# Kernel optimization log

Measured on AMD Instinct MI355X. Metric: run time of the kernel, lower is better.

## Reference

```python
import jax, jax.numpy as jnp
import numpy as np

EMBED_DIM = 1024
NUM_HEADS = 16
HEAD_DIM = EMBED_DIM // NUM_HEADS


def setup_inputs() -> dict:
    key = jax.random.key(0)
    ks = jax.random.split(key, 5)
    B, N, E = 2, 2048, EMBED_DIM
    scale = E ** -0.5
    return {
        "x": jax.random.normal(ks[0], (B, N, E), dtype=jnp.float32),
        "w_qkv": jax.random.normal(ks[1], (E, 3 * E), dtype=jnp.float32) * scale,
        "b_qkv": jnp.zeros((3 * E,), dtype=jnp.float32),
        "w_proj": jax.random.normal(ks[2], (E, E), dtype=jnp.float32) * scale,
        "b_proj": jnp.zeros((E,), dtype=jnp.float32),
    }


def reference(x, w_qkv, b_qkv, w_proj, b_proj):
    B, N, E = x.shape
    H, D = NUM_HEADS, HEAD_DIM
    qkv = x @ w_qkv + b_qkv                      # [B,N,3E]
    qkv = qkv.reshape(B, N, 3, H, D)
    q = qkv[:, :, 0].transpose(0, 2, 1, 3)        # [B,H,N,D]
    k = qkv[:, :, 1].transpose(0, 2, 1, 3)
    v = qkv[:, :, 2].transpose(0, 2, 1, 3)
    attn = jnp.einsum('bhnd,bhmd->bhnm', q, k) * (D ** -0.5)
    attn = jax.nn.softmax(attn, axis=-1)          # dropout is identity in eval mode
    out = jnp.einsum('bhnm,bhmd->bhnd', attn, v)  # [B,H,N,D]
    out = out.transpose(0, 2, 1, 3).reshape(B, N, E)
    return out @ w_proj + b_proj
```

## Files before the change

### kernel.cpp

```cpp
#include <hip/hip_runtime.h>
#include <hip/hip_bf16.h>
#include <cstdint>
#include <cstddef>


typedef __attribute__((ext_vector_type(8))) short short8;
typedef __attribute__((ext_vector_type(4))) short short4v;
typedef __attribute__((ext_vector_type(4))) float f32x4;

#define MFMA16(a, b, c) __builtin_amdgcn_mfma_f32_16x16x32_bf16((a), (b), (c), 0, 0, 0)

__device__ __forceinline__ float b2f(short s) {
  union { unsigned u; float f; } x; x.u = ((unsigned)(unsigned short)s) << 16; return x.f;
}
__device__ __forceinline__ short f2b(float f) {
  union { float f; unsigned u; } x; x.f = f;
  unsigned r = x.u + 0x7fffu + ((x.u >> 16) & 1u);
  return (short)(r >> 16);
}
__device__ __forceinline__ void async_lds16(const void* g, void* l) {
  __builtin_amdgcn_global_load_lds(
      (const __attribute__((address_space(1))) void*)g,
      (__attribute__((address_space(3))) void*)l, 16, 0, 0);
}

__global__ __launch_bounds__(256) void cast_f32_bf16(const float* __restrict__ in,
                                                     short* __restrict__ out, int n4) {
  int idx = blockIdx.x * 256 + threadIdx.x;
  if (idx < n4) {
    f32x4 v = ((const f32x4*)in)[idx];
    short4v o;
    #pragma unroll
    for (int e = 0; e < 4; ++e) o[e] = f2b(v[e]);
    ((short4v*)out)[idx] = o;
  }
}

__global__ __launch_bounds__(256) void transpose_cast(const float* __restrict__ in,
                                                      short* __restrict__ out,
                                                      int R, int C) {
  __shared__ float tile[32][33];
  int c0 = blockIdx.x * 32, r0 = blockIdx.y * 32;
  int tx = threadIdx.x, ty = threadIdx.y;
  #pragma unroll
  for (int i = ty; i < 32; i += 8)
    tile[i][tx] = in[(size_t)(r0 + i) * C + c0 + tx];
  __syncthreads();
  #pragma unroll
  for (int i = ty; i < 32; i += 8)
    out[(size_t)(c0 + i) * R + r0 + tx] = f2b(tile[tx][i]);
}

__global__ __launch_bounds__(256) void gemm_qkv(const short* __restrict__ xb,
                                                const short* __restrict__ wT,
                                                const float* __restrict__ bias,
                                                short* __restrict__ Qb,
                                                short* __restrict__ Kb,
                                                short* __restrict__ Vt) {
  __shared__ short lds_a[128 * 32];
  __shared__ short lds_b[128 * 32];
  const int tid = threadIdx.x, wid = tid >> 6, lane = tid & 63;
  const int lg = lane >> 4, lr = lane & 15;
  const int m0 = blockIdx.x * 128, n0 = blockIdx.y * 128;
  const int wr = wid >> 1, wc = wid & 1;
  const int K = 1024;

  f32x4 acc[4][4];
  #pragma unroll
  for (int i = 0; i < 4; ++i)
    #pragma unroll
    for (int j = 0; j < 4; ++j) acc[i][j] = (f32x4)0.0f;

  for (int k0 = 0; k0 < K; k0 += 32) {
    #pragma unroll
    for (int it = 0; it < 2; ++it) {
      int chunk = it * 256 + tid;
      int row = chunk >> 2, kc = (chunk & 3) * 8;
      async_lds16(xb + (size_t)(m0 + row) * K + k0 + kc, lds_a + chunk * 8);
      async_lds16(wT + (size_t)(n0 + row) * K + k0 + kc, lds_b + chunk * 8);
    }
    __syncthreads();
    short8 af[4], bfr[4];
    #pragma unroll
    for (int i = 0; i < 4; ++i)
      af[i] = *(const short8*)&lds_a[(wr * 64 + i * 16 + lr) * 32 + lg * 8];
    #pragma unroll
    for (int j = 0; j < 4; ++j)
      bfr[j] = *(const short8*)&lds_b[(wc * 64 + j * 16 + lr) * 32 + lg * 8];
    #pragma unroll
    for (int i = 0; i < 4; ++i)
      #pragma unroll
      for (int j = 0; j < 4; ++j) acc[i][j] = MFMA16(af[i], bfr[j], acc[i][j]);
    __syncthreads();
  }

  #pragma unroll
  for (int i = 0; i < 4; ++i) {
    int gm = m0 + wr * 64 + i * 16 + lg * 4;
    int bb = gm >> 11, n = gm & 2047;
    #pragma unroll
    for (int j = 0; j < 4; ++j) {
      int gc = n0 + wc * 64 + j * 16 + lr;
      float bv = bias[gc];
      int which = gc >> 10;
      int h = (gc >> 6) & 15;
      int dd = gc & 63;
      size_t qkbase = ((size_t)((bb * 16 + h) * 2048 + n)) * 64 + dd;
      if (which == 2) {
        size_t vtbase = ((size_t)((bb * 16 + h) * 64 + dd)) * 2048 + n;
        short4v pv;
        #pragma unroll
        for (int r = 0; r < 4; ++r) pv[r] = f2b(acc[i][j][r] + bv);
        *(short4v*)&Vt[vtbase] = pv;
      } else {
        short* dst = (which == 0) ? Qb : Kb;
        #pragma unroll
        for (int r = 0; r < 4; ++r)
          dst[qkbase + (size_t)r * 64] = f2b(acc[i][j][r] + bv);
      }
    }
  }
}

__global__ __launch_bounds__(512) void attn_fwd(const short* __restrict__ Qb,
                                                const short* __restrict__ Kb,
                                                const short* __restrict__ Vt,
                                                short* __restrict__ aob) {
  __shared__ short k_lds[64 * 64];
  __shared__ short v_lds[64 * 64];
  __shared__ short p_lds[8 * 16 * 64];
  const int tid = threadIdx.x, wid = tid >> 6, lane = tid & 63;
  const int lg = lane >> 4, lr = lane & 15;
  const int bh = blockIdx.x, qt = blockIdx.y;
  const int q0 = qt * 128 + wid * 16;
  const short* Qbh = Qb + (size_t)bh * 2048 * 64;
  const short* Kbh = Kb + (size_t)bh * 2048 * 64;
  const short* Vbh = Vt + (size_t)bh * 64 * 2048;
  const int rm = (lr >> 1) & 7;

  short8 qf[2];
  #pragma unroll
  for (int kk = 0; kk < 2; ++kk) {
    qf[kk] = *(const short8*)(Qbh + (size_t)(q0 + lr) * 64 + kk * 32 + lg * 8);
    #pragma unroll
    for (int e = 0; e < 8; ++e) qf[kk][e] = f2b(b2f(qf[kk][e]) * 0.125f);
  }

  f32x4 o[4];
  #pragma unroll
  for (int dt = 0; dt < 4; ++dt) o[dt] = (f32x4)0.0f;
  float m_ = -__builtin_inff(), l_ = 0.0f;

  for (int kv0 = 0; kv0 < 2048; kv0 += 64) {
    {
      int row = tid >> 3;
      int src = ((tid & 7) ^ ((row >> 1) & 7)) * 8;
      async_lds16(Kbh + (size_t)(kv0 + row) * 64 + src, k_lds + tid * 8);
      async_lds16(Vbh + (size_t)row * 2048 + kv0 + src, v_lds + tid * 8);
    }
    __syncthreads();

    f32x4 s[4];
    #pragma unroll
    for (int jt = 0; jt < 4; ++jt) s[jt] = (f32x4)0.0f;
    #pragma unroll
    for (int jt = 0; jt < 4; ++jt)
      #pragma unroll
      for (int kk = 0; kk < 2; ++kk) {
        short8 kf = *(const short8*)&k_lds[(jt * 16 + lr) * 64 +
                                           (((kk * 4 + lg) ^ rm) * 8)];
        s[jt] = MFMA16(kf, qf[kk], s[jt]);
      }

    float mx = s[0][0];
    #pragma unroll
    for (int jt = 0; jt < 4; ++jt)
      #pragma unroll
      for (int r = 0; r < 4; ++r) mx = fmaxf(mx, s[jt][r]);
    mx = fmaxf(mx, __shfl_xor(mx, 16));
    mx = fmaxf(mx, __shfl_xor(mx, 32));
    float mn = fmaxf(m_, mx);
    float corr = __expf(m_ - mn);
    m_ = mn;
    float ps = 0.0f;
    #pragma unroll
    for (int jt = 0; jt < 4; ++jt)
      #pragma unroll
      for (int r = 0; r < 4; ++r) {
        float p = __expf(s[jt][r] - mn);
        s[jt][r] = p;
        ps += p;
      }
    ps += __shfl_xor(ps, 16);
    ps += __shfl_xor(ps, 32);
    l_ = l_ * corr + ps;
    #pragma unroll
    for (int dt = 0; dt < 4; ++dt)
      #pragma unroll
      for (int r = 0; r < 4; ++r) o[dt][r] *= corr;

    #pragma unroll
    for (int jt = 0; jt < 4; ++jt) {
      short4v pv;
      #pragma unroll
      for (int r = 0; r < 4; ++r) pv[r] = f2b(s[jt][r]);
      *(short4v*)&p_lds[wid * 1024 + lr * 64 +
                        (((jt * 2 + (lg >> 1)) ^ rm) * 8) + (lg & 1) * 4] = pv;
    }
    asm volatile("s_waitcnt lgkmcnt(0)" ::: "memory");
    __builtin_amdgcn_sched_barrier(0);

    #pragma unroll
    for (int kk = 0; kk < 2; ++kk) {
      short8 pa = *(const short8*)&p_lds[wid * 1024 + lr * 64 +
                                         (((kk * 4 + lg) ^ rm) * 8)];
      #pragma unroll
      for (int dt = 0; dt < 4; ++dt) {
        short8 vb = *(const short8*)&v_lds[(dt * 16 + lr) * 64 +
                                           (((kk * 4 + lg) ^ rm) * 8)];
        o[dt] = MFMA16(vb, pa, o[dt]);
      }
    }
    __syncthreads();
  }

  const int bb = bh >> 4, h = bh & 15;
  const float inv_l = __frcp_rn(l_);
  #pragma unroll
  for (int dt = 0; dt < 4; ++dt) {
    short4v ov;
    #pragma unroll
    for (int r = 0; r < 4; ++r) ov[r] = f2b(o[dt][r] * inv_l);
    *(short4v*)&aob[(size_t)(bb * 2048 + q0 + lr) * 1024 + h * 64 + dt * 16 + lg * 4] = ov;
  }
}

__global__ __launch_bounds__(256) void gemm_proj(const short* __restrict__ aob,
                                                 const short* __restrict__ wT,
                                                 const float* __restrict__ bias,
                                                 float* __restrict__ out) {
  __shared__ short lds_a[128 * 32];
  __shared__ short lds_b[128 * 32];
  const int tid = threadIdx.x, wid = tid >> 6, lane = tid & 63;
  const int lg = lane >> 4, lr = lane & 15;
  const int m0 = blockIdx.x * 128, n0 = blockIdx.y * 128;
  const int wr = wid >> 1, wc = wid & 1;
  const int K = 1024;

  f32x4 acc[4][4];
  #pragma unroll
  for (int i = 0; i < 4; ++i)
    #pragma unroll
    for (int j = 0; j < 4; ++j) acc[i][j] = (f32x4)0.0f;

  for (int k0 = 0; k0 < K; k0 += 32) {
    #pragma unroll
    for (int it = 0; it < 2; ++it) {
      int chunk = it * 256 + tid;
      int row = chunk >> 2, kc = (chunk & 3) * 8;
      async_lds16(aob + (size_t)(m0 + row) * K + k0 + kc, lds_a + chunk * 8);
      async_lds16(wT + (size_t)(n0 + row) * K + k0 + kc, lds_b + chunk * 8);
    }
    __syncthreads();
    short8 af[4], bfr[4];
    #pragma unroll
    for (int i = 0; i < 4; ++i)
      af[i] = *(const short8*)&lds_a[(wr * 64 + i * 16 + lr) * 32 + lg * 8];
    #pragma unroll
    for (int j = 0; j < 4; ++j)
      bfr[j] = *(const short8*)&lds_b[(wc * 64 + j * 16 + lr) * 32 + lg * 8];
    #pragma unroll
    for (int i = 0; i < 4; ++i)
      #pragma unroll
      for (int j = 0; j < 4; ++j) acc[i][j] = MFMA16(af[i], bfr[j], acc[i][j]);
    __syncthreads();
  }

  #pragma unroll
  for (int i = 0; i < 4; ++i) {
    int gm = m0 + wr * 64 + i * 16 + lg * 4;
    #pragma unroll
    for (int j = 0; j < 4; ++j) {
      int gc = n0 + wc * 64 + j * 16 + lr;
      float bv = bias[gc];
      #pragma unroll
      for (int r = 0; r < 4; ++r)
        out[(size_t)(gm + r) * 1024 + gc] = acc[i][j][r] + bv;
    }
  }
}

extern "C" void kernel_launch(void* const* d_in, const int* in_sizes, int n_in,
                              void* d_out, int out_size, void* d_ws, size_t ws_size,
                              hipStream_t stream) {
  const float* x     = (const float*)d_in[0];
  const float* wqkv  = (const float*)d_in[1];
  const float* bqkv  = (const float*)d_in[2];
  const float* wproj = (const float*)d_in[3];
  const float* bproj = (const float*)d_in[4];
  float* out = (float*)d_out;

  char* ws = (char*)d_ws;
  short* xb     = (short*)ws; ws += (size_t)4096 * 1024 * 2;
  short* wqkvT  = (short*)ws; ws += (size_t)3072 * 1024 * 2;
  short* wprojT = (short*)ws; ws += (size_t)1024 * 1024 * 2;
  short* Qb     = (short*)ws; ws += (size_t)32 * 2048 * 64 * 2;
  short* Kb     = (short*)ws; ws += (size_t)32 * 2048 * 64 * 2;
  short* Vt     = (short*)ws; ws += (size_t)32 * 64 * 2048 * 2;
  short* aob    = (short*)ws; ws += (size_t)4096 * 1024 * 2;

  cast_f32_bf16<<<4096, 256, 0, stream>>>(x, xb, 4096 * 1024 / 4);
  transpose_cast<<<dim3(96, 32), dim3(32, 8), 0, stream>>>(wqkv, wqkvT, 1024, 3072);
  transpose_cast<<<dim3(32, 32), dim3(32, 8), 0, stream>>>(wproj, wprojT, 1024, 1024);
  gemm_qkv<<<dim3(32, 24), 256, 0, stream>>>(xb, wqkvT, bqkv, Qb, Kb, Vt);
  attn_fwd<<<dim3(32, 16), 512, 0, stream>>>(Qb, Kb, Vt, aob);
  gemm_proj<<<dim3(32, 8), 256, 0, stream>>>(aob, wprojT, bproj, out);
}
```

Baseline: 221.8 us.

## Double-buffer attention K/V, use exp2 with lazy rescale, swizzle blocks, shrink proj tile

The attention kernel now double-buffers the K/V tiles in LDS so the next tile's async load overlaps compute. Softmax uses exp2 with log2e folded into the Q scale, and the running max is only rescaled when it grows by more than a threshold. All three GEMM/attention kernels remap block IDs with an XCD-style swizzle, and the projection GEMM uses 64x128 tiles to launch more blocks. These target memory-load latency, transcendental cost, and load balance across XCDs, at the cost of more LDS and some numerical slack from deferred rescaling.

New measurement: 214.5 us. 3.3% less time.

```diff
diff --git a/kernel.cpp b/kernel.cpp
--- a/kernel.cpp
+++ b/kernel.cpp
@@ -9,6 +9,7 @@
 typedef __attribute__((ext_vector_type(4))) float f32x4;
 
 #define MFMA16(a, b, c) __builtin_amdgcn_mfma_f32_16x16x32_bf16((a), (b), (c), 0, 0, 0)
+#define EXP2F(x) __builtin_amdgcn_exp2f(x)
 
 __device__ __forceinline__ float b2f(short s) {
   union { unsigned u; float f; } x; x.u = ((unsigned)(unsigned short)s) << 16; return x.f;
@@ -61,7 +62,9 @@
   __shared__ short lds_b[128 * 32];
   const int tid = threadIdx.x, wid = tid >> 6, lane = tid & 63;
   const int lg = lane >> 4, lr = lane & 15;
-  const int m0 = blockIdx.x * 128, n0 = blockIdx.y * 128;
+  const int lin = blockIdx.x;
+  const int swz = (lin & 7) * 96 + (lin >> 3);
+  const int m0 = (swz & 31) * 128, n0 = (swz >> 5) * 128;
   const int wr = wid >> 1, wc = wid & 1;
   const int K = 1024;
 
@@ -126,24 +129,29 @@
                                                 const short* __restrict__ Kb,
                                                 const short* __restrict__ Vt,
                                                 short* __restrict__ aob) {
-  __shared__ short k_lds[64 * 64];
-  __shared__ short v_lds[64 * 64];
+  __shared__ short k_lds[2][64 * 64];
+  __shared__ short v_lds[2][64 * 64];
   __shared__ short p_lds[8 * 16 * 64];
   const int tid = threadIdx.x, wid = tid >> 6, lane = tid & 63;
   const int lg = lane >> 4, lr = lane & 15;
-  const int bh = blockIdx.x, qt = blockIdx.y;
+  const int lin = blockIdx.x;
+  const int swz = (lin & 7) * 64 + (lin >> 3);
+  const int qt = swz & 15, bh = swz >> 4;
   const int q0 = qt * 128 + wid * 16;
   const short* Qbh = Qb + (size_t)bh * 2048 * 64;
   const short* Kbh = Kb + (size_t)bh * 2048 * 64;
   const short* Vbh = Vt + (size_t)bh * 64 * 2048;
   const int rm = (lr >> 1) & 7;
 
+  const int srow = tid >> 3;
+  const int ssrc = ((tid & 7) ^ ((srow >> 1) & 7)) * 8;
+
   short8 qf[2];
   #pragma unroll
   for (int kk = 0; kk < 2; ++kk) {
     qf[kk] = *(const short8*)(Qbh + (size_t)(q0 + lr) * 64 + kk * 32 + lg * 8);
     #pragma unroll
-    for (int e = 0; e < 8; ++e) qf[kk][e] = f2b(b2f(qf[kk][e]) * 0.125f);
+    for (int e = 0; e < 8; ++e) qf[kk][e] = f2b(b2f(qf[kk][e]) * 0.1803368801f);
   }
 
   f32x4 o[4];
@@ -151,14 +159,18 @@
   for (int dt = 0; dt < 4; ++dt) o[dt] = (f32x4)0.0f;
   float m_ = -__builtin_inff(), l_ = 0.0f;
 
-  for (int kv0 = 0; kv0 < 2048; kv0 += 64) {
-    {
-      int row = tid >> 3;
-      int src = ((tid & 7) ^ ((row >> 1) & 7)) * 8;
-      async_lds16(Kbh + (size_t)(kv0 + row) * 64 + src, k_lds + tid * 8);
-      async_lds16(Vbh + (size_t)row * 2048 + kv0 + src, v_lds + tid * 8);
-    }
-    __syncthreads();
+  async_lds16(Kbh + (size_t)srow * 64 + ssrc, &k_lds[0][tid * 8]);
+  async_lds16(Vbh + (size_t)srow * 2048 + 0 + ssrc, &v_lds[0][tid * 8]);
+  asm volatile("s_waitcnt vmcnt(0)" ::: "memory");
+  __syncthreads();
+
+  for (int t = 0; t < 32; ++t) {
+    const int cur = t & 1;
+    if (t + 1 < 32) {
+      int kvn = (t + 1) * 64;
+      async_lds16(Kbh + (size_t)(kvn + srow) * 64 + ssrc, &k_lds[cur ^ 1][tid * 8]);
+      async_lds16(Vbh + (size_t)srow * 2048 + kvn + ssrc, &v_lds[cur ^ 1][tid * 8]);
+    }
 
     f32x4 s[4];
     #pragma unroll
@@ -167,37 +179,40 @@
     for (int jt = 0; jt < 4; ++jt)
       #pragma unroll
       for (int kk = 0; kk < 2; ++kk) {
-        short8 kf = *(const short8*)&k_lds[(jt * 16 + lr) * 64 +
-                                           (((kk * 4 + lg) ^ rm) * 8)];
+        short8 kf = *(const short8*)&k_lds[cur][(jt * 16 + lr) * 64 +
+                                               (((kk * 4 + lg) ^ rm) * 8)];
         s[jt] = MFMA16(kf, qf[kk], s[jt]);
       }
 
-    float mx = s[0][0];
+    float pmax = s[0][0];
     #pragma unroll
     for (int jt = 0; jt < 4; ++jt)
       #pragma unroll
-      for (int r = 0; r < 4; ++r) mx = fmaxf(mx, s[jt][r]);
-    mx = fmaxf(mx, __shfl_xor(mx, 16));
-    mx = fmaxf(mx, __shfl_xor(mx, 32));
-    float mn = fmaxf(m_, mx);
-    float corr = __expf(m_ - mn);
-    m_ = mn;
+      for (int r = 0; r < 4; ++r) pmax = fmaxf(pmax, s[jt][r]);
+    pmax = fmaxf(pmax, __shfl_xor(pmax, 16));
+    pmax = fmaxf(pmax, __shfl_xor(pmax, 32));
+    if (!__all(pmax - m_ <= 8.0f)) {
+      float mn = fmaxf(m_, pmax);
+      float corr = EXP2F(m_ - mn);
+      m_ = mn;
+      l_ *= corr;
+      #pragma unroll
+      for (int dt = 0; dt < 4; ++dt)
+        #pragma unroll
+        for (int r = 0; r < 4; ++r) o[dt][r] *= corr;
+    }
     float ps = 0.0f;
     #pragma unroll
     for (int jt = 0; jt < 4; ++jt)
       #pragma unroll
       for (int r = 0; r < 4; ++r) {
-        float p = __expf(s[jt][r] - mn);
+        float p = EXP2F(s[jt][r] - m_);
         s[jt][r] = p;
         ps += p;
       }
     ps += __shfl_xor(ps, 16);
     ps += __shfl_xor(ps, 32);
-    l_ = l_ * corr + ps;
-    #pragma unroll
-    for (int dt = 0; dt < 4; ++dt)
-      #pragma unroll
-      for (int r = 0; r < 4; ++r) o[dt][r] *= corr;
+    l_ += ps;
 
     #pragma unroll
     for (int jt = 0; jt < 4; ++jt) {
@@ -216,11 +231,12 @@
                                          (((kk * 4 + lg) ^ rm) * 8)];
       #pragma unroll
       for (int dt = 0; dt < 4; ++dt) {
-        short8 vb = *(const short8*)&v_lds[(dt * 16 + lr) * 64 +
-                                           (((kk * 4 + lg) ^ rm) * 8)];
+        short8 vb = *(const short8*)&v_lds[cur][(dt * 16 + lr) * 64 +
+                                               (((kk * 4 + lg) ^ rm) * 8)];
         o[dt] = MFMA16(vb, pa, o[dt]);
       }
     }
+    asm volatile("s_waitcnt vmcnt(0)" ::: "memory");
     __syncthreads();
   }
 
@@ -239,49 +255,54 @@
                                                  const short* __restrict__ wT,
                                                  const float* __restrict__ bias,
                                                  float* __restrict__ out) {
-  __shared__ short lds_a[128 * 32];
+  __shared__ short lds_a[64 * 32];
   __shared__ short lds_b[128 * 32];
   const int tid = threadIdx.x, wid = tid >> 6, lane = tid & 63;
   const int lg = lane >> 4, lr = lane & 15;
-  const int m0 = blockIdx.x * 128, n0 = blockIdx.y * 128;
-  const int wr = wid >> 1, wc = wid & 1;
+  const int lin = blockIdx.x;
+  const int swz = (lin & 7) * 64 + (lin >> 3);
+  const int m0 = (swz & 63) * 64, n0 = (swz >> 6) * 128;
+  const int mw = wid >> 1, nw = wid & 1;
   const int K = 1024;
 
-  f32x4 acc[4][4];
-  #pragma unroll
-  for (int i = 0; i < 4; ++i)
+  f32x4 acc[2][4];
+  #pragma unroll
+  for (int i = 0; i < 2; ++i)
     #pragma unroll
     for (int j = 0; j < 4; ++j) acc[i][j] = (f32x4)0.0f;
 
   for (int k0 = 0; k0 < K; k0 += 32) {
+    {
+      int row = tid >> 2, kc = (tid & 3) * 8;
+      async_lds16(aob + (size_t)(m0 + row) * K + k0 + kc, lds_a + tid * 8);
+    }
     #pragma unroll
     for (int it = 0; it < 2; ++it) {
       int chunk = it * 256 + tid;
       int row = chunk >> 2, kc = (chunk & 3) * 8;
-      async_lds16(aob + (size_t)(m0 + row) * K + k0 + kc, lds_a + chunk * 8);
       async_lds16(wT + (size_t)(n0 + row) * K + k0 + kc, lds_b + chunk * 8);
     }
     __syncthreads();
-    short8 af[4], bfr[4];
-    #pragma unroll
-    for (int i = 0; i < 4; ++i)
-      af[i] = *(const short8*)&lds_a[(wr * 64 + i * 16 + lr) * 32 + lg * 8];
+    short8 af[2], bfr[4];
+    #pragma unroll
+    for (int i = 0; i < 2; ++i)
+      af[i] = *(const short8*)&lds_a[(mw * 32 + i * 16 + lr) * 32 + lg * 8];
     #pragma unroll
     for (int j = 0; j < 4; ++j)
-      bfr[j] = *(const short8*)&lds_b[(wc * 64 + j * 16 + lr) * 32 + lg * 8];
-    #pragma unroll
-    for (int i = 0; i < 4; ++i)
+      bfr[j] = *(const short8*)&lds_b[(nw * 64 + j * 16 + lr) * 32 + lg * 8];
+    #pragma unroll
+    for (int i = 0; i < 2; ++i)
       #pragma unroll
       for (int j = 0; j < 4; ++j) acc[i][j] = MFMA16(af[i], bfr[j], acc[i][j]);
     __syncthreads();
   }
 
   #pragma unroll
-  for (int i = 0; i < 4; ++i) {
-    int gm = m0 + wr * 64 + i * 16 + lg * 4;
+  for (int i = 0; i < 2; ++i) {
+    int gm = m0 + mw * 32 + i * 16 + lg * 4;
     #pragma unroll
     for (int j = 0; j < 4; ++j) {
-      int gc = n0 + wc * 64 + j * 16 + lr;
+      int gc = n0 + nw * 64 + j * 16 + lr;
       float bv = bias[gc];
       #pragma unroll
       for (int r = 0; r < 4; ++r)
@@ -312,7 +333,7 @@
   cast_f32_bf16<<<4096, 256, 0, stream>>>(x, xb, 4096 * 1024 / 4);
   transpose_cast<<<dim3(96, 32), dim3(32, 8), 0, stream>>>(wqkv, wqkvT, 1024, 3072);
   transpose_cast<<<dim3(32, 32), dim3(32, 8), 0, stream>>>(wproj, wprojT, 1024, 1024);
-  gemm_qkv<<<dim3(32, 24), 256, 0, stream>>>(xb, wqkvT, bqkv, Qb, Kb, Vt);
-  attn_fwd<<<dim3(32, 16), 512, 0, stream>>>(Qb, Kb, Vt, aob);
-  gemm_proj<<<dim3(32, 8), 256, 0, stream>>>(aob, wprojT, bproj, out);
-}
+  gemm_qkv<<<768, 256, 0, stream>>>(xb, wqkvT, bqkv, Qb, Kb, Vt);
+  attn_fwd<<<512, 512, 0, stream>>>(Qb, Kb, Vt, aob);
+  gemm_proj<<<512, 256, 0, stream>>>(aob, wprojT, bproj, out);
+}
```
